# Kernel tuning notes

Hardware: AMD Instinct MI355X
Metric: run time of the kernel (lower is better)

The kernel has to match this reference:

```python
import jax, jax.numpy as jnp
import numpy as np

THR_CONF = 0.05
THR_NMS = 0.5
TOPK = 500


def _pairwise_iou(b):
    # b: [M,4] ltrb
    lt = jnp.maximum(b[:, None, :2], b[None, :, :2])
    rb = jnp.minimum(b[:, None, 2:], b[None, :, 2:])
    wh = jnp.clip(rb - lt, 0.0)
    inter = wh[..., 0] * wh[..., 1]
    area = (b[:, 2] - b[:, 0]) * (b[:, 3] - b[:, 1])
    union = area[:, None] + area[None, :] - inter
    return inter / jnp.maximum(union, 1e-9)


def _greedy_nms(boxes_off, scores, valid, thr):
    # fixed-size greedy NMS matching torchvision.ops.nms semantics
    M = boxes_off.shape[0]
    neg = jnp.finfo(scores.dtype).min
    s = jnp.where(valid, scores, neg)
    order = jnp.argsort(-s)
    iou = _pairwise_iou(boxes_off[order])  # [M,M]
    valid_o = valid[order]
    rng = jnp.arange(M)

    def body(i, keep):
        sup = (iou[i] > thr) & (rng > i) & keep[i]
        return keep & ~sup

    keep_o = jax.lax.fori_loop(0, M, body, valid_o)
    keep = jnp.zeros((M,), dtype=bool).at[order].set(keep_o)
    return keep


def setup_inputs() -> dict:
    key = jax.random.key(0)
    k1, k2 = jax.random.split(key)
    B, N, C = 8, 40000, 80
    pconf = jax.random.normal(k1, (B, N, C), dtype=jnp.float32)
    raw = jax.random.uniform(k2, (B, N, 4), dtype=jnp.float32)
    cxcy = raw[..., :2]
    wh = raw[..., 2:] * 0.2 + 0.01
    pboxes = jnp.concatenate([cxcy - wh / 2, cxcy + wh / 2], axis=-1)  # ltrb
    return {"pconf": pconf, "pboxes": pboxes}


def reference(pconf, pboxes):
    B, N, C = pconf.shape
    conf = jax.nn.sigmoid(pconf)
    pscores = conf.max(axis=-1)          # [B,N]
    plabels = conf.argmax(axis=-1)       # [B,N]

    mask_pos = pscores > THR_CONF
    # topk mask via scatter (mirrors mask_topk[arange[:,None], ids_topk] = True)
    scores_k, ids_topk = jax.lax.top_k(pscores, TOPK)       # [B,K]
    mask_topk = jnp.zeros_like(mask_pos)
    mask_topk = mask_topk.at[jnp.arange(B)[:, None], ids_topk].set(True)
    mask_pos = mask_pos & mask_topk

    # gather stage-1 results at the topk positions (fixed size B*K)
    valid_k = jnp.take_along_axis(mask_pos, ids_topk, axis=1)              # [B,K]
    labels_k = jnp.take_along_axis(plabels, ids_topk, axis=1)              # [B,K]
    boxes_k = jnp.take_along_axis(pboxes, ids_topk[..., None], axis=1)     # [B,K,4]

    M = B * TOPK
    ids_batch1 = jnp.repeat(jnp.arange(B), TOPK)            # [M]
    p_scores1 = scores_k.reshape(M)
    p_labels1 = labels_k.reshape(M)
    p_boxes1 = boxes_k.reshape(M, 4)
    valid1 = valid_k.reshape(M)

    # per-(label,batch) offset trick == per-label loop of batched_nms
    max_coord = p_boxes1.max()
    key = (p_labels1 * B + ids_batch1).astype(p_boxes1.dtype)
    boxes_off = p_boxes1 + (key * (max_coord + 1.0))[:, None]

    keep = _greedy_nms(boxes_off, p_scores1, valid1, THR_NMS)

    return (ids_batch1, p_boxes1, p_labels1, p_scores1, keep)
```

## Files before the change

### kernel.cpp

```cpp
#include <hip/hip_runtime.h>
#include <math.h>

#define BB 8
#define NN 40000
#define CC 80
#define TOPK 500
#define MM (BB*TOPK)
#define NBINS 4096
#define BIN_LO (-8.0f)
#define BIN_SCALE 256.0f
#define CAP 4096
#define NGROUPS (CC*BB)
#define THR_CONF_F 0.05f
#define THR_NMS_F 0.5f

__device__ __forceinline__ int bin_of(float x){
  float f = (x - BIN_LO) * BIN_SCALE;
  int b = (int)floorf(f);
  b = b < 0 ? 0 : b;
  b = b > (NBINS-1) ? (NBINS-1) : b;
  return b;
}

__global__ void k_score(const float* __restrict__ pconf,
                        float* __restrict__ logitv, int* __restrict__ label){
  int g   = blockIdx.x*256 + threadIdx.x;
  int row = g >> 2;
  int sub = g & 3;
  const float4* p = (const float4*)pconf + (size_t)row*20 + sub;
  float4 v0 = p[0], v1 = p[4], v2 = p[8], v3 = p[12], v4 = p[16];
  float best = -3.4e38f; int bi = 0;
  int c0 = sub*4;
  #define CHK(vv,it) { \
    int base = c0 + (it)*16; \
    if(vv.x>best){best=vv.x;bi=base+0;} \
    if(vv.y>best){best=vv.y;bi=base+1;} \
    if(vv.z>best){best=vv.z;bi=base+2;} \
    if(vv.w>best){best=vv.w;bi=base+3;} }
  CHK(v0,0) CHK(v1,1) CHK(v2,2) CHK(v3,3) CHK(v4,4)
  #undef CHK
  #pragma unroll
  for(int d=1; d<4; d<<=1){
    float ov = __shfl_xor(best, d, 64);
    int   oi = __shfl_xor(bi,   d, 64);
    if(ov > best || (ov == best && oi < bi)){ best = ov; bi = oi; }
  }
  if(sub == 0){
    logitv[row] = best; label[row] = bi;
  }
}

__global__ void __launch_bounds__(1024)
k_histthresh(const float* __restrict__ logitv, int* __restrict__ tbin){
  int b = blockIdx.x;
  int t = threadIdx.x;
  __shared__ int h[NBINS];
  __shared__ int ss[1024];
  for(int i=t; i<NBINS; i+=1024) h[i] = 0;
  __syncthreads();
  const float4* lv4 = (const float4*)(logitv + (size_t)b*NN);
  for(int i=t; i<NN/4; i+=1024){
    float4 v = lv4[i];
    atomicAdd(&h[bin_of(v.x)], 1);
    atomicAdd(&h[bin_of(v.y)], 1);
    atomicAdd(&h[bin_of(v.z)], 1);
    atomicAdd(&h[bin_of(v.w)], 1);
  }
  __syncthreads();
  int c0 = t*4;
  int cs = h[c0] + h[c0+1] + h[c0+2] + h[c0+3];
  ss[t] = cs;
  __syncthreads();
  for(int off=1; off<1024; off<<=1){
    int v = (t+off < 1024) ? ss[t+off] : 0;
    __syncthreads();
    ss[t] += v;
    __syncthreads();
  }
  int sufExcl = (t < 1023) ? ss[t+1] : 0;
  if(sufExcl < TOPK && sufExcl + cs >= TOPK){
    int cum = sufExcl; int tb = 0;
    for(int k=3; k>=0; k--){
      cum += h[c0+k];
      if(cum >= TOPK){ tb = c0+k; break; }
    }
    tb -= 2; if(tb < 0) tb = 0;
    tbin[b] = tb;
  }
}

__global__ void k_compact(const float* __restrict__ logitv,
                          const int* __restrict__ tbin, int* __restrict__ cnt,
                          unsigned long long* __restrict__ cand){
  int row = blockIdx.x*256 + threadIdx.x;
  if(row >= BB*NN) return;
  int b = row / NN;
  float lg = logitv[row];
  if(bin_of(lg) >= tbin[b]){
    int pos = atomicAdd(&cnt[b], 1);
    if(pos < CAP){
      float t = (float)exp(-(double)lg);
      float s = 1.0f/(1.0f+t);
      unsigned int sb = __float_as_uint(s);
      int idx = row - b*NN;
      cand[(size_t)b*CAP + pos] =
        ((unsigned long long)sb << 16) | (unsigned long long)(65535 - idx);
    }
  }
}

__global__ void __launch_bounds__(512)
k_rankemit(const unsigned long long* __restrict__ cand, const int* __restrict__ cnt,
           const int* __restrict__ label, const float* __restrict__ pboxes,
           float* __restrict__ out,
           float* __restrict__ cbox, int* __restrict__ cgid,
           float* __restrict__ cscore, int* __restrict__ maxbits){
  int b = blockIdx.x;
  __shared__ unsigned long long keys[CAP];
  int n = cnt[b]; if(n > CAP) n = CAP;
  for(int i=threadIdx.x; i<n; i+=512) keys[i] = cand[(size_t)b*CAP + i];
  __syncthreads();
  for(int i=threadIdx.x; i<n; i+=512){
    unsigned long long ki = keys[i];
    int rank = 0;
    for(int j=0; j<n; j++) rank += (keys[j] > ki) ? 1 : 0;
    if(rank < TOPK){
      int idx = 65535 - (int)(ki & 0xFFFFULL);
      int row = b*NN + idx;
      float s = __uint_as_float((unsigned int)(ki >> 16));
      int lab = label[row];
      float4 bv = *(const float4*)(pboxes + (size_t)row*4);
      int m = b*TOPK + rank;
      out[m] = (float)b;
      float* ob = out + MM + (size_t)m*4;
      ob[0]=bv.x; ob[1]=bv.y; ob[2]=bv.z; ob[3]=bv.w;
      out[5*MM + m] = (float)lab;
      out[6*MM + m] = s;
      cbox[m*4+0]=bv.x; cbox[m*4+1]=bv.y; cbox[m*4+2]=bv.z; cbox[m*4+3]=bv.w;
      cgid[m] = lab*BB + b;
      cscore[m] = s;
      float mx = fmaxf(fmaxf(bv.x,bv.y), fmaxf(bv.z,bv.w));
      atomicMax(maxbits, __float_as_int(mx));
    }
  }
}

__global__ void __launch_bounds__(64)
k_nms(const float* __restrict__ cbox, const int* __restrict__ cgid,
      const float* __restrict__ cscore, const int* __restrict__ maxbits,
      float* __restrict__ out_keep){
  int g = blockIdx.x;
  int lane = threadIdx.x;
  __shared__ float bx[TOPK][4];
  __shared__ float area[TOPK];
  __shared__ int   mid[TOPK];
  __shared__ unsigned char keepf[TOPK];
  float mc  = __int_as_float(*maxbits);
  float off = (float)g * (mc + 1.0f);
  int b = g & (BB-1);
  int lo = b*TOPK, hi = lo + TOPK;

  int count = 0;
  for(int base=lo; base<hi; base+=64){
    int m = base + lane;
    bool match = (m < hi) && (cgid[m] == g);
    unsigned long long mk = __ballot(match);
    if(match){
      int p = count + __popcll(mk & ((1ULL<<lane)-1ULL));
      float x1 = cbox[m*4+0] + off;
      float y1 = cbox[m*4+1] + off;
      float x2 = cbox[m*4+2] + off;
      float y2 = cbox[m*4+3] + off;
      bx[p][0]=x1; bx[p][1]=y1; bx[p][2]=x2; bx[p][3]=y2;
      area[p] = (x2-x1)*(y2-y1);
      mid[p] = m;
      keepf[p] = (cscore[m] > THR_CONF_F) ? 1 : 0;
    }
    count += __popcll(mk);
  }
  __syncthreads();

  for(int i=0; i<count; i++){
    if(keepf[i]){
      float ix1=bx[i][0], iy1=bx[i][1], ix2=bx[i][2], iy2=bx[i][3], ia=area[i];
      for(int j=i+1+lane; j<count; j+=64){
        if(keepf[j]){
          float lx = fmaxf(ix1, bx[j][0]);
          float ly = fmaxf(iy1, bx[j][1]);
          float rx = fminf(ix2, bx[j][2]);
          float ry = fminf(iy2, bx[j][3]);
          float w = fmaxf(rx-lx, 0.0f), h = fmaxf(ry-ly, 0.0f);
          float inter = w*h;
          float uni = ia + area[j] - inter;
          float iou = inter / fmaxf(uni, 1e-9f);
          if(iou > THR_NMS_F) keepf[j] = 0;
        }
      }
    }
    __syncthreads();
  }
  for(int p=lane; p<count; p+=64)
    out_keep[mid[p]] = keepf[p] ? 1.0f : 0.0f;
}

extern "C" void kernel_launch(void* const* d_in, const int* in_sizes, int n_in,
                              void* d_out, int out_size, void* d_ws, size_t ws_size,
                              hipStream_t stream) {
  const float* pconf  = (const float*)d_in[0];
  const float* pboxes = (const float*)d_in[1];
  float* out = (float*)d_out;
  char* ws = (char*)d_ws;

  int* cnt     = (int*)(ws + 0);
  int* maxbits = (int*)(ws + 32);
  int* tbin    = (int*)(ws + 64);
  float* logitv  = (float*)(ws + 128);
  int*   label   = (int*)  (ws + 1280128);
  unsigned long long* cand = (unsigned long long*)(ws + 2560128);
  float* cbox   = (float*)(ws + 2822272);
  int*   cgid   = (int*)  (ws + 2886272);
  float* cscore = (float*)(ws + 2902272);

  hipMemsetAsync(ws, 0, 64, stream);

  k_score     <<<(BB*NN*4)/256, 256, 0, stream>>>(pconf, logitv, label);
  k_histthresh<<<BB, 1024, 0, stream>>>(logitv, tbin);
  k_compact   <<<(BB*NN+255)/256, 256, 0, stream>>>(logitv, tbin, cnt, cand);
  k_rankemit  <<<BB, 512, 0, stream>>>(cand, cnt, label, pboxes, out,
                                       cbox, cgid, cscore, maxbits);
  k_nms       <<<NGROUPS, 64, 0, stream>>>(cbox, cgid, cscore, maxbits, out + 7*MM);
}
```

Baseline: 238.3 us.

## Fuse histogram threshold, compaction and ranking into one per-batch kernel

Merges the histogram-threshold, candidate-compaction and rank/emit kernels into a single per-batch kernel that keeps the threshold, candidate keys and counters in shared memory. It also removes the memset and the global atomics by writing a per-batch max that the NMS kernel reduces itself. This removes two kernel launches, the memset, and the global round-trips for candidate data. In exchange the compaction pass now runs on only 8 blocks rather than a full grid, and ranking uses 1024 threads per block.

```diff
diff --git a/kernel.cpp b/kernel.cpp
--- a/kernel.cpp
+++ b/kernel.cpp
@@ -51,13 +51,21 @@
 }
 
 __global__ void __launch_bounds__(1024)
-k_histthresh(const float* __restrict__ logitv, int* __restrict__ tbin){
+k_select(const float* __restrict__ logitv, const int* __restrict__ label,
+         const float* __restrict__ pboxes,
+         float* __restrict__ out,
+         float* __restrict__ cbox, int* __restrict__ cgid,
+         float* __restrict__ cscore, int* __restrict__ maxval){
   int b = blockIdx.x;
   int t = threadIdx.x;
   __shared__ int h[NBINS];
   __shared__ int ss[1024];
+  __shared__ unsigned long long keys[CAP];
+  __shared__ int stbin, scnt, smax;
   for(int i=t; i<NBINS; i+=1024) h[i] = 0;
-  __syncthreads();
+  if(t==0){ scnt = 0; smax = 0; }
+  __syncthreads();
+
   const float4* lv4 = (const float4*)(logitv + (size_t)b*NN);
   for(int i=t; i<NN/4; i+=1024){
     float4 v = lv4[i];
@@ -67,6 +75,7 @@
     atomicAdd(&h[bin_of(v.w)], 1);
   }
   __syncthreads();
+
   int c0 = t*4;
   int cs = h[c0] + h[c0+1] + h[c0+2] + h[c0+3];
   ss[t] = cs;
@@ -85,42 +94,28 @@
       if(cum >= TOPK){ tb = c0+k; break; }
     }
     tb -= 2; if(tb < 0) tb = 0;
-    tbin[b] = tb;
-  }
-}
-
-__global__ void k_compact(const float* __restrict__ logitv,
-                          const int* __restrict__ tbin, int* __restrict__ cnt,
-                          unsigned long long* __restrict__ cand){
-  int row = blockIdx.x*256 + threadIdx.x;
-  if(row >= BB*NN) return;
-  int b = row / NN;
-  float lg = logitv[row];
-  if(bin_of(lg) >= tbin[b]){
-    int pos = atomicAdd(&cnt[b], 1);
-    if(pos < CAP){
-      float t = (float)exp(-(double)lg);
-      float s = 1.0f/(1.0f+t);
-      unsigned int sb = __float_as_uint(s);
-      int idx = row - b*NN;
-      cand[(size_t)b*CAP + pos] =
-        ((unsigned long long)sb << 16) | (unsigned long long)(65535 - idx);
-    }
-  }
-}
-
-__global__ void __launch_bounds__(512)
-k_rankemit(const unsigned long long* __restrict__ cand, const int* __restrict__ cnt,
-           const int* __restrict__ label, const float* __restrict__ pboxes,
-           float* __restrict__ out,
-           float* __restrict__ cbox, int* __restrict__ cgid,
-           float* __restrict__ cscore, int* __restrict__ maxbits){
-  int b = blockIdx.x;
-  __shared__ unsigned long long keys[CAP];
-  int n = cnt[b]; if(n > CAP) n = CAP;
-  for(int i=threadIdx.x; i<n; i+=512) keys[i] = cand[(size_t)b*CAP + i];
-  __syncthreads();
-  for(int i=threadIdx.x; i<n; i+=512){
+    stbin = tb;
+  }
+  __syncthreads();
+  int tb = stbin;
+
+  const float* lv = logitv + (size_t)b*NN;
+  for(int idx=t; idx<NN; idx+=1024){
+    float lg = lv[idx];
+    if(bin_of(lg) >= tb){
+      int pos = atomicAdd(&scnt, 1);
+      if(pos < CAP){
+        float e = (float)exp(-(double)lg);
+        float s = 1.0f/(1.0f+e);
+        keys[pos] = ((unsigned long long)__float_as_uint(s) << 16)
+                  | (unsigned long long)(65535 - idx);
+      }
+    }
+  }
+  __syncthreads();
+  int n = scnt; if(n > CAP) n = CAP;
+
+  for(int i=t; i<n; i+=1024){
     unsigned long long ki = keys[i];
     int rank = 0;
     for(int j=0; j<n; j++) rank += (keys[j] > ki) ? 1 : 0;
@@ -140,14 +135,16 @@
       cgid[m] = lab*BB + b;
       cscore[m] = s;
       float mx = fmaxf(fmaxf(bv.x,bv.y), fmaxf(bv.z,bv.w));
-      atomicMax(maxbits, __float_as_int(mx));
-    }
-  }
+      atomicMax(&smax, __float_as_int(mx));
+    }
+  }
+  __syncthreads();
+  if(t==0) maxval[b] = smax;
 }
 
 __global__ void __launch_bounds__(64)
 k_nms(const float* __restrict__ cbox, const int* __restrict__ cgid,
-      const float* __restrict__ cscore, const int* __restrict__ maxbits,
+      const float* __restrict__ cscore, const int* __restrict__ maxval,
       float* __restrict__ out_keep){
   int g = blockIdx.x;
   int lane = threadIdx.x;
@@ -155,7 +152,10 @@
   __shared__ float area[TOPK];
   __shared__ int   mid[TOPK];
   __shared__ unsigned char keepf[TOPK];
-  float mc  = __int_as_float(*maxbits);
+  int mb = maxval[0];
+  #pragma unroll
+  for(int k=1;k<BB;k++) mb = max(mb, maxval[k]);
+  float mc  = __int_as_float(mb);
   float off = (float)g * (mc + 1.0f);
   int b = g & (BB-1);
   int lo = b*TOPK, hi = lo + TOPK;
@@ -211,22 +211,15 @@
   float* out = (float*)d_out;
   char* ws = (char*)d_ws;
 
-  int* cnt     = (int*)(ws + 0);
-  int* maxbits = (int*)(ws + 32);
-  int* tbin    = (int*)(ws + 64);
-  float* logitv  = (float*)(ws + 128);
-  int*   label   = (int*)  (ws + 1280128);
-  unsigned long long* cand = (unsigned long long*)(ws + 2560128);
-  float* cbox   = (float*)(ws + 2822272);
-  int*   cgid   = (int*)  (ws + 2886272);
-  float* cscore = (float*)(ws + 2902272);
-
-  hipMemsetAsync(ws, 0, 64, stream);
-
-  k_score     <<<(BB*NN*4)/256, 256, 0, stream>>>(pconf, logitv, label);
-  k_histthresh<<<BB, 1024, 0, stream>>>(logitv, tbin);
-  k_compact   <<<(BB*NN+255)/256, 256, 0, stream>>>(logitv, tbin, cnt, cand);
-  k_rankemit  <<<BB, 512, 0, stream>>>(cand, cnt, label, pboxes, out,
-                                       cbox, cgid, cscore, maxbits);
-  k_nms       <<<NGROUPS, 64, 0, stream>>>(cbox, cgid, cscore, maxbits, out + 7*MM);
-}
+  float* logitv  = (float*)(ws + 0);
+  int*   label   = (int*)  (ws + 1280000);
+  float* cbox    = (float*)(ws + 2560000);
+  int*   cgid    = (int*)  (ws + 2624000);
+  float* cscore  = (float*)(ws + 2640000);
+  int*   maxval  = (int*)  (ws + 2656000);
+
+  k_score <<<(BB*NN*4)/256, 256, 0, stream>>>(pconf, logitv, label);
+  k_select<<<BB, 1024, 0, stream>>>(logitv, label, pboxes, out,
+                                    cbox, cgid, cscore, maxval);
+  k_nms   <<<NGROUPS, 64, 0, stream>>>(cbox, cgid, cscore, maxval, out + 7*MM);
+}
```

After: 191.0 us. -19.8%, faster.
